# Optimization experiments

Measured on AMD Instinct MI355X. Metric: run time of the kernel, lower is better.

The kernel has to match this reference:

```python
import jax, jax.numpy as jnp
import numpy as np

EPS = 1e-5

def setup_inputs() -> dict:
    key = jax.random.key(0)
    ks = jax.random.split(key, 5)
    B, C, N, L = 32, 128, 4096, 6
    M = N // 8  # 512
    x = jax.random.normal(ks[0], (B, C, N, 1), dtype=jnp.float32)
    # small init scale keeps softmax logits in a sane range
    W_pool = jax.random.normal(ks[1], (M, C), dtype=jnp.float32) * 0.05
    Wf = jax.random.normal(ks[2], (L, M, M), dtype=jnp.float32) * 0.02
    gamma = jnp.ones((L, M), dtype=jnp.float32)
    beta = jnp.zeros((L, M), dtype=jnp.float32)
    W_unpool = jax.random.normal(ks[3], (M, C), dtype=jnp.float32) * 0.05
    b_unpool = jnp.zeros((M,), dtype=jnp.float32)
    return {"x": x, "W_pool": W_pool, "Wf": Wf, "gamma": gamma,
            "beta": beta, "W_unpool": W_unpool, "b_unpool": b_unpool}


def reference(x, W_pool, Wf, gamma, beta, W_unpool, b_unpool):
    # x: [B, C, N, 1]
    xs = x[..., 0]  # [B, C, N]
    # ---- Pool_1_to_1: 1x1 conv C->M, softmax over N, weighted sum ----
    Spool = jax.nn.softmax(jnp.einsum('mc,bcn->bmn', W_pool, xs), axis=2)
    h = jnp.einsum('bcn,bmn->bmc', xs, Spool)  # pooled then transposed: [B, M, C]
    # ---- n_layers of Order_Aware_Filtering_1_to_1 on [B, M, C] (channels=M) ----
    L = Wf.shape[0]
    for l in range(L):
        y = jnp.einsum('om,bmc->boc', Wf[l], h)  # 1x1 conv M->M
        mu = jnp.mean(y, axis=(0, 2), keepdims=True)          # BN over (B, spatial)
        var = jnp.mean((y - mu) ** 2, axis=(0, 2), keepdims=True)  # biased var
        yn = (y - mu) * jax.lax.rsqrt(var + EPS)
        yn = yn * gamma[l][None, :, None] + beta[l][None, :, None]
        h = jax.nn.relu(yn + h)  # residual + non-lin
    x1 = jnp.transpose(h, (0, 2, 1))  # [B, C, M]
    # ---- Unpool_1_to_1: 1x1 conv (with bias) C->M, softmax over M ----
    ul = jnp.einsum('mc,bcn->bmn', W_unpool, xs) + b_unpool[None, :, None]
    Sun = jax.nn.softmax(ul, axis=1)
    out = jnp.einsum('bcm,bmn->bcn', x1, Sun)
    return out[..., None]  # [B, C, N, 1]
```

## Files before the change

kernel.cpp:

```cpp
#include <hip/hip_runtime.h>
#include <hip/hip_bf16.h>

typedef float f32x4 __attribute__((ext_vector_type(4)));
typedef __bf16 bf16_t;
typedef __bf16 bf16x4 __attribute__((ext_vector_type(4)));
typedef __bf16 bf16x8 __attribute__((ext_vector_type(8)));

#define MFMA16(a, b, c) __builtin_amdgcn_mfma_f32_16x16x32_bf16(a, b, c, 0, 0, 0)

constexpr int C_ = 128;
constexpr int N_ = 4096;
constexpr int M_ = 512;
constexpr int NL = 6;

#define NEG_INF (-__builtin_huge_valf())

constexpr int XST = 136;
constexpr int NSTP = 40;
constexpr int PSTU = 72;

__global__ __launch_bounds__(256) void k_wsplit(const float* __restrict__ W,
                                                bf16_t* __restrict__ hi,
                                                bf16_t* __restrict__ lo) {
  const size_t i4 = ((size_t)blockIdx.x * 256 + threadIdx.x) * 4;
  f32x4 v = *(const f32x4*)&W[i4];
  bf16x4 h4, l4;
#pragma unroll
  for (int k = 0; k < 4; ++k) {
    bf16_t h = (bf16_t)v[k];
    h4[k] = h;
    l4[k] = (bf16_t)(v[k] - (float)h);
  }
  *(bf16x4*)&hi[i4] = h4;
  *(bf16x4*)&lo[i4] = l4;
}

__global__ __launch_bounds__(256) void k_wfsplit(const float* __restrict__ W,
                                                 bf16_t* __restrict__ hi,
                                                 bf16_t* __restrict__ lo) {
  const size_t i4 = ((size_t)blockIdx.x * 256 + threadIdx.x) * 4;
  const int l = (int)(i4 >> 18);
  const int rem = (int)(i4 & 262143);
  const int o = rem >> 9, m = rem & 511;
  f32x4 v = *(const f32x4*)&W[i4];
  bf16x4 h4, l4;
#pragma unroll
  for (int k = 0; k < 4; ++k) {
    bf16_t h = (bf16_t)v[k];
    h4[k] = h;
    l4[k] = (bf16_t)(v[k] - (float)h);
  }
  const size_t ad = (((size_t)l * 16 + (m >> 5)) * 512 + o) * 32 + (m & 31);
  *(bf16x4*)&hi[ad] = h4;
  *(bf16x4*)&lo[ad] = l4;
}

__global__ __launch_bounds__(256) void k_wusplit(const float* __restrict__ W,
                                                 bf16_t* __restrict__ hi,
                                                 bf16_t* __restrict__ lo) {
  const size_t i4 = ((size_t)blockIdx.x * 256 + threadIdx.x) * 4;
  const int m = (int)(i4 >> 7), c = (int)(i4 & 127);
  f32x4 v = *(const f32x4*)&W[i4];
  bf16x4 h4, l4;
#pragma unroll
  for (int k = 0; k < 4; ++k) {
    bf16_t h = (bf16_t)v[k];
    h4[k] = h;
    l4[k] = (bf16_t)(v[k] - (float)h);
  }
  const size_t ad = ((size_t)(c >> 5) * 512 + m) * 32 + (c & 31);
  *(bf16x4*)&hi[ad] = h4;
  *(bf16x4*)&lo[ad] = l4;
}

__global__ __launch_bounds__(256) void k_xsplit(const float* __restrict__ xs,
                                                bf16_t* __restrict__ thi,
                                                bf16_t* __restrict__ tlo) {
  __shared__ float T[128 * 68];
  const int n0 = blockIdx.x * 64, b = blockIdx.y;
  const int t = threadIdx.x;
  const float* xsb = xs + (size_t)b * C_ * N_;
#pragma unroll
  for (int i = 0; i < 8; ++i) {
    int slot = i * 256 + t;
    int c = slot >> 4, n4 = (slot & 15) * 4;
    *(f32x4*)&T[c * 68 + n4] = *(const f32x4*)&xsb[(size_t)c * N_ + n0 + n4];
  }
  __syncthreads();
  const int n = t >> 2, cb = (t & 3) * 32;
  bf16x8 h8[4], l8[4];
#pragma unroll
  for (int g = 0; g < 4; ++g)
#pragma unroll
    for (int j = 0; j < 8; ++j) {
      float v = T[(cb + g * 8 + j) * 68 + n];
      bf16_t hh = (bf16_t)v;
      h8[g][j] = hh;
      l8[g][j] = (bf16_t)(v - (float)hh);
    }
  const size_t base = ((size_t)b * N_ + n0 + n) * C_ + cb;
#pragma unroll
  for (int g = 0; g < 4; ++g) {
    *(bf16x8*)&thi[base + g * 8] = h8[g];
    *(bf16x8*)&tlo[base + g * 8] = l8[g];
  }
}

__global__ __launch_bounds__(256) void k_pool(const bf16_t* __restrict__ xsThi,
                                              const bf16_t* __restrict__ xsTlo,
                                              const float* __restrict__ x,
                                              const bf16_t* __restrict__ Wph,
                                              const bf16_t* __restrict__ Wpl,
                                              float* __restrict__ h_part,
                                              float* __restrict__ ml) {
  __shared__ bf16_t XH[32 * XST], XL[32 * XST];
  __shared__ bf16_t XCH[128 * NSTP], XCL[128 * NSTP];
  const int d = blockIdx.x;
  const int lin = ((d & 7) << 7) | (d >> 3);
  const int b = lin >> 5, r5 = lin & 31;
  const int mt = r5 >> 2, seg = r5 & 3;
  const int m0 = mt * 64;
  const int t = threadIdx.x, w = t >> 6, lane = t & 63, l15 = lane & 15, q = lane >> 4;

  const int sn0 = t >> 4, sn1 = (256 + t) >> 4;
  const int scg = (t & 15) * 8;
  const size_t sgb = ((size_t)b * N_ + seg * 1024) * C_ + scg;
  const int xc = t >> 3, xn4 = (t & 7) * 4;
  const float* xb = x + (size_t)b * C_ * N_;

  bf16x8 aWh[4], aWl[4];
#pragma unroll
  for (int k = 0; k < 4; ++k) {
    const size_t ra = (size_t)(m0 + w * 16 + l15) * C_ + k * 32 + q * 8;
    aWh[k] = *(const bf16x8*)&Wph[ra];
    aWl[k] = *(const bf16x8*)&Wpl[ra];
  }

  f32x4 acc[8];
#pragma unroll
  for (int cs = 0; cs < 8; ++cs) acc[cs] = f32x4{0.f, 0.f, 0.f, 0.f};
  float lsum = 0.f;

  for (int ch = 0; ch < 32; ++ch) {
    const int n0g = seg * 1024 + ch * 32;
    const size_t off = sgb + (size_t)ch * 32 * C_;
    __syncthreads();
    bf16x8 th0 = *(const bf16x8*)&xsThi[off + (size_t)sn0 * C_];
    bf16x8 th1 = *(const bf16x8*)&xsThi[off + (size_t)sn1 * C_];
    bf16x8 tl0 = *(const bf16x8*)&xsTlo[off + (size_t)sn0 * C_];
    bf16x8 tl1 = *(const bf16x8*)&xsTlo[off + (size_t)sn1 * C_];
    f32x4 xv[4];
#pragma unroll
    for (int i = 0; i < 4; ++i) {
      const int c = xc + i * 32;
      xv[i] = *(const f32x4*)&xb[(size_t)c * N_ + n0g + xn4];
    }
    *(bf16x8*)&XH[sn0 * XST + scg] = th0;
    *(bf16x8*)&XH[sn1 * XST + scg] = th1;
    *(bf16x8*)&XL[sn0 * XST + scg] = tl0;
    *(bf16x8*)&XL[sn1 * XST + scg] = tl1;
#pragma unroll
    for (int i = 0; i < 4; ++i) {
      const int c = xc + i * 32;
      bf16x4 h4, l4;
#pragma unroll
      for (int j = 0; j < 4; ++j) {
        bf16_t hh = (bf16_t)xv[i][j];
        h4[j] = hh;
        l4[j] = (bf16_t)(xv[i][j] - (float)hh);
      }
      *(bf16x4*)&XCH[c * NSTP + xn4] = h4;
      *(bf16x4*)&XCL[c * NSTP + xn4] = l4;
    }
    __syncthreads();

    f32x4 U0 = f32x4{0.f, 0.f, 0.f, 0.f}, U1 = f32x4{0.f, 0.f, 0.f, 0.f};
#pragma unroll
    for (int k = 0; k < 4; ++k) {
      {
        const int o = l15 * XST + k * 32 + q * 8;
        bf16x8 bh = *(const bf16x8*)&XH[o];
        bf16x8 bl = *(const bf16x8*)&XL[o];
        U0 = MFMA16(bh, aWh[k], U0);
        U0 = MFMA16(bl, aWh[k], U0);
        U0 = MFMA16(bh, aWl[k], U0);
      }
      {
        const int o = (16 + l15) * XST + k * 32 + q * 8;
        bf16x8 bh = *(const bf16x8*)&XH[o];
        bf16x8 bl = *(const bf16x8*)&XL[o];
        U1 = MFMA16(bh, aWh[k], U1);
        U1 = MFMA16(bl, aWh[k], U1);
        U1 = MFMA16(bh, aWl[k], U1);
      }
    }

    f32x4 pe0, pe1;
#pragma unroll
    for (int r = 0; r < 4; ++r) {
      pe0[r] = __expf(U0[r]);
      pe1[r] = __expf(U1[r]);
      lsum += pe0[r] + pe1[r];
    }

    const int slo = l15 + ((lane & 16) ? 32 : 0);
    float pj[8];
#pragma unroll
    for (int r = 0; r < 4; ++r) {
      float a0 = __shfl(pe0[r], slo);
      float a1 = __shfl(pe1[r], slo);
      pj[r] = (q & 2) ? a1 : a0;
      float b0 = __shfl(pe0[r], slo + 16);
      float b1 = __shfl(pe1[r], slo + 16);
      pj[4 + r] = (q & 2) ? b1 : b0;
    }
    bf16x8 aPh, aPl;
#pragma unroll
    for (int j = 0; j < 8; ++j) {
      bf16_t hh = (bf16_t)pj[j];
      aPh[j] = hh;
      aPl[j] = (bf16_t)(pj[j] - (float)hh);
    }

#pragma unroll
    for (int cs = 0; cs < 8; ++cs) {
      const int ob = (cs * 16 + l15) * NSTP + q * 8;
      bf16x8 bh = *(const bf16x8*)&XCH[ob];
      bf16x8 bl = *(const bf16x8*)&XCL[ob];
      acc[cs] = MFMA16(aPh, bh, acc[cs]);
      acc[cs] = MFMA16(aPh, bl, acc[cs]);
      acc[cs] = MFMA16(aPl, bh, acc[cs]);
    }
  }

  const size_t sb = (size_t)seg * 32 + b;
  lsum += __shfl_xor(lsum, 16);
  lsum += __shfl_xor(lsum, 32);
  if (lane < 16) ml[sb * 512 + m0 + w * 16 + lane] = lsum;
#pragma unroll
  for (int cs = 0; cs < 8; ++cs)
#pragma unroll
    for (int r = 0; r < 4; ++r) {
      const int m = m0 + w * 16 + q * 4 + r;
      h_part[(sb * 512 + m) * 128 + cs * 16 + l15] = acc[cs][r];
    }
}

__global__ __launch_bounds__(128) void k_combine(const float* __restrict__ h_part,
                                                 const float* __restrict__ ml,
                                                 float* __restrict__ hbuf) {
  const int mb = blockIdx.x;
  const int m = mb >> 5, b = mb & 31;
  const int c = threadIdx.x;
  float L = 0.f, acc = 0.f;
#pragma unroll
  for (int s = 0; s < 4; ++s) {
    L += ml[((size_t)s * 32 + b) * 512 + m];
    acc += h_part[(((size_t)s * 32 + b) * 512 + m) * 128 + c];
  }
  hbuf[(size_t)m * 4096 + b * 128 + c] = acc / L;
}

__global__ __launch_bounds__(256) void k_hsplit(const float* __restrict__ h,
                                                bf16_t* __restrict__ thi,
                                                bf16_t* __restrict__ tlo) {
  __shared__ float T[64 * 65];
  const int m0 = blockIdx.x * 64, c0 = blockIdx.y * 64;
  const int t = threadIdx.x;
#pragma unroll
  for (int ii = 0; ii < 4; ++ii) {
    int slot = ii * 256 + t;
    int m = slot >> 4, c4 = (slot & 15) * 4;
    f32x4 v = *(const f32x4*)&h[(size_t)(m0 + m) * 4096 + c0 + c4];
#pragma unroll
    for (int k = 0; k < 4; ++k) T[(c4 + k) * 65 + m] = v[k];
  }
  __syncthreads();
  const int row = t >> 2, mg = (t & 3) * 16;
  const int bc = c0 + row, bb = bc >> 7, cc = bc & 127;
#pragma unroll
  for (int half = 0; half < 2; ++half) {
    bf16x8 h8, l8;
#pragma unroll
    for (int j = 0; j < 8; ++j) {
      float v = T[row * 65 + mg + half * 8 + j];
      bf16_t hh = (bf16_t)v;
      h8[j] = hh;
      l8[j] = (bf16_t)(v - (float)hh);
    }
    const int m8 = m0 + mg + half * 8;
    const size_t ad = (((size_t)bb * 16 + (m8 >> 5)) * 128 + cc) * 32 + (m8 & 31);
    *(bf16x8*)&thi[ad] = h8;
    *(bf16x8*)&tlo[ad] = l8;
  }
}

__global__ __launch_bounds__(256) void k_bnsplit(const float* __restrict__ ybuf,
                                                 float* __restrict__ hbuf,
                                                 const float* __restrict__ stats,
                                                 const float* __restrict__ gamma,
                                                 const float* __restrict__ beta,
                                                 int l,
                                                 bf16_t* __restrict__ thi,
                                                 bf16_t* __restrict__ tlo) {
  __shared__ float T[64 * 65];
  const int m0 = blockIdx.x * 64, c0 = blockIdx.y * 64;
  const int t = threadIdx.x;
#pragma unroll
  for (int ii = 0; ii < 4; ++ii) {
    int slot = ii * 256 + t;
    int m = slot >> 4, c4 = (slot & 15) * 4;
    const int o = m0 + m;
    const float mu = stats[l * 1024 + o] * (1.f / 4096.f);
    const float var = stats[l * 1024 + 512 + o] * (1.f / 4096.f) - mu * mu;
    const float rs = rsqrtf(var + 1e-5f);
    const float g = gamma[l * 512 + o];
    const float bt = beta[l * 512 + o];
    const size_t gidx = (size_t)o * 4096 + c0 + c4;
    f32x4 y = *(const f32x4*)&ybuf[gidx];
    f32x4 h = *(const f32x4*)&hbuf[gidx];
    f32x4 r;
#pragma unroll
    for (int k = 0; k < 4; ++k) {
      r[k] = fmaxf((y[k] - mu) * rs * g + bt + h[k], 0.f);
      T[(c4 + k) * 65 + m] = r[k];
    }
    *(f32x4*)&hbuf[gidx] = r;
  }
  __syncthreads();
  const int row = t >> 2, mg = (t & 3) * 16;
  const int bc = c0 + row, bb = bc >> 7, cc = bc & 127;
#pragma unroll
  for (int half = 0; half < 2; ++half) {
    bf16x8 h8, l8;
#pragma unroll
    for (int j = 0; j < 8; ++j) {
      float v = T[row * 65 + mg + half * 8 + j];
      bf16_t hh = (bf16_t)v;
      h8[j] = hh;
      l8[j] = (bf16_t)(v - (float)hh);
    }
    const int m8 = m0 + mg + half * 8;
    const size_t ad = (((size_t)bb * 16 + (m8 >> 5)) * 128 + cc) * 32 + (m8 & 31);
    *(bf16x8*)&thi[ad] = h8;
    *(bf16x8*)&tlo[ad] = l8;
  }
}

__global__ __launch_bounds__(256) void k_layerA(const bf16_t* __restrict__ Whi,
                                                const bf16_t* __restrict__ Wlo,
                                                const bf16_t* __restrict__ hThi,
                                                const bf16_t* __restrict__ hTlo,
                                                int l, float* __restrict__ ybuf,
                                                float* __restrict__ stats) {
  const int o0 = blockIdx.x * 32;
  const int bb = blockIdx.y;
  const int t = threadIdx.x;
  const int w = t >> 6, lane = t & 63, l15 = lane & 15, q = lane >> 4;
  const int bcw = bb * 128 + w * 32;

  f32x4 acc[2][2];
#pragma unroll
  for (int i = 0; i < 2; ++i)
#pragma unroll
    for (int j = 0; j < 2; ++j) acc[i][j] = f32x4{0.f, 0.f, 0.f, 0.f};

  for (int k0 = 0; k0 < M_; k0 += 32) {
    const int mb = k0 >> 5;
    bf16x8 ah[2], al[2], bh[2], bl[2];
#pragma unroll
    for (int os = 0; os < 2; ++os) {
      const size_t ro =
          (((size_t)l * 16 + mb) * 512 + o0 + os * 16 + l15) * 32 + q * 8;
      ah[os] = *(const bf16x8*)&Whi[ro];
      al[os] = *(const bf16x8*)&Wlo[ro];
    }
#pragma unroll
    for (int ns = 0; ns < 2; ++ns) {
      const size_t rb =
          (((size_t)bb * 16 + mb) * 128 + w * 32 + ns * 16 + l15) * 32 + q * 8;
      bh[ns] = *(const bf16x8*)&hThi[rb];
      bl[ns] = *(const bf16x8*)&hTlo[rb];
    }
#pragma unroll
    for (int os = 0; os < 2; ++os)
#pragma unroll
      for (int ns = 0; ns < 2; ++ns) {
        acc[os][ns] = MFMA16(ah[os], bh[ns], acc[os][ns]);
        acc[os][ns] = MFMA16(ah[os], bl[ns], acc[os][ns]);
        acc[os][ns] = MFMA16(al[os], bh[ns], acc[os][ns]);
      }
  }

  float s1[2][4], s2[2][4];
#pragma unroll
  for (int os = 0; os < 2; ++os)
#pragma unroll
    for (int r = 0; r < 4; ++r) {
      float a = 0.f, b2 = 0.f;
#pragma unroll
      for (int ns = 0; ns < 2; ++ns) {
        float v = acc[os][ns][r];
        ybuf[(size_t)(o0 + os * 16 + q * 4 + r) * 4096 + bcw + ns * 16 + l15] = v;
        a += v;
        b2 += v * v;
      }
      s1[os][r] = a;
      s2[os][r] = b2;
    }
#pragma unroll
  for (int os = 0; os < 2; ++os)
#pragma unroll
    for (int r = 0; r < 4; ++r) {
#pragma unroll
      for (int off = 1; off < 16; off <<= 1) {
        s1[os][r] += __shfl_xor(s1[os][r], off);
        s2[os][r] += __shfl_xor(s2[os][r], off);
      }
      if (l15 == 0) {
        const int o = o0 + os * 16 + q * 4 + r;
        atomicAdd(&stats[l * 1024 + o], s1[os][r]);
        atomicAdd(&stats[l * 1024 + 512 + o], s2[os][r]);
      }
    }
}

__global__ __launch_bounds__(256) void k_unpool(const bf16_t* __restrict__ xsThi,
                                                const bf16_t* __restrict__ xsTlo,
                                                const bf16_t* __restrict__ Wuh,
                                                const bf16_t* __restrict__ Wul,
                                                const float* __restrict__ bun,
                                                const bf16_t* __restrict__ x1hi,
                                                const bf16_t* __restrict__ x1lo,
                                                float* __restrict__ out) {
  __shared__ bf16_t XH[64 * XST], XL[64 * XST];
  __shared__ bf16_t PH[64 * PSTU], PL[64 * PSTU];
  __shared__ float colsum_s[4][64];
  __shared__ float L_s[64];
  const int n0 = blockIdx.x * 64, b = blockIdx.y;
  const int t = threadIdx.x, w = t >> 6, lane = t & 63, l15 = lane & 15, q = lane >> 4;

#pragma unroll
  for (int i = 0; i < 4; ++i) {
    int slot = i * 256 + t;
    int n = slot >> 4, cg = (slot & 15) * 8;
    const size_t g = ((size_t)b * N_ + n0 + n) * C_ + cg;
    *(bf16x8*)&XH[n * XST + cg] = *(const bf16x8*)&xsThi[g];
    *(bf16x8*)&XL[n * XST + cg] = *(const bf16x8*)&xsTlo[g];
  }
  colsum_s[w][lane] = 0.f;
  f32x4 acc[2][4];
#pragma unroll
  for (int cs = 0; cs < 2; ++cs)
#pragma unroll
    for (int nt = 0; nt < 4; ++nt) acc[cs][nt] = f32x4{0.f, 0.f, 0.f, 0.f};
  __syncthreads();

  for (int ch = 0; ch < 8; ++ch) {
    const int mg0 = ch * 64 + w * 16;
    f32x4 U[4];
#pragma unroll
    for (int nt = 0; nt < 4; ++nt) U[nt] = f32x4{0.f, 0.f, 0.f, 0.f};
#pragma unroll
    for (int k = 0; k < 4; ++k) {
      const size_t ra = ((size_t)k * 512 + mg0 + l15) * 32 + q * 8;
      bf16x8 ah = *(const bf16x8*)&Wuh[ra];
      bf16x8 al = *(const bf16x8*)&Wul[ra];
#pragma unroll
      for (int nt = 0; nt < 4; ++nt) {
        const int o = (nt * 16 + l15) * XST + k * 32 + q * 8;
        bf16x8 bh = *(const bf16x8*)&XH[o];
        bf16x8 bl = *(const bf16x8*)&XL[o];
        U[nt] = MFMA16(ah, bh, U[nt]);
        U[nt] = MFMA16(ah, bl, U[nt]);
        U[nt] = MFMA16(al, bh, U[nt]);
      }
    }
    float bi[4];
#pragma unroll
    for (int r = 0; r < 4; ++r) bi[r] = bun[mg0 + q * 4 + r];

#pragma unroll
    for (int nt = 0; nt < 4; ++nt) {
      bf16x4 ph4, pl4;
      float s = 0.f;
#pragma unroll
      for (int r = 0; r < 4; ++r) {
        float pv = __expf(U[nt][r] + bi[r]);
        s += pv;
        bf16_t hh = (bf16_t)pv;
        ph4[r] = hh;
        pl4[r] = (bf16_t)(pv - (float)hh);
      }
      s += __shfl_xor(s, 16);
      s += __shfl_xor(s, 32);
      if (lane < 16) colsum_s[w][nt * 16 + lane] += s;
      const int o = (nt * 16 + l15) * PSTU + w * 16 + q * 4;
      *(bf16x4*)&PH[o] = ph4;
      *(bf16x4*)&PL[o] = pl4;
    }
    __syncthreads();

#pragma unroll
    for (int ks = 0; ks < 2; ++ks) {
      bf16x8 ah2[2], al2[2];
#pragma unroll
      for (int cs = 0; cs < 2; ++cs) {
        const size_t ga =
            (((size_t)b * 16 + ch * 2 + ks) * 128 + w * 32 + cs * 16 + l15) * 32 +
            q * 8;
        ah2[cs] = *(const bf16x8*)&x1hi[ga];
        al2[cs] = *(const bf16x8*)&x1lo[ga];
      }
#pragma unroll
      for (int nt = 0; nt < 4; ++nt) {
        const int o = (nt * 16 + l15) * PSTU + ks * 32 + q * 8;
        bf16x8 bh = *(const bf16x8*)&PH[o];
        bf16x8 bl = *(const bf16x8*)&PL[o];
#pragma unroll
        for (int cs = 0; cs < 2; ++cs) {
          acc[cs][nt] = MFMA16(ah2[cs], bh, acc[cs][nt]);
          acc[cs][nt] = MFMA16(ah2[cs], bl, acc[cs][nt]);
          acc[cs][nt] = MFMA16(al2[cs], bh, acc[cs][nt]);
        }
      }
    }
    __syncthreads();
  }
  if (t < 64)
    L_s[t] = colsum_s[0][t] + colsum_s[1][t] + colsum_s[2][t] + colsum_s[3][t];
  __syncthreads();
#pragma unroll
  for (int nt = 0; nt < 4; ++nt) {
    const float invL = 1.f / L_s[nt * 16 + l15];
#pragma unroll
    for (int cs = 0; cs < 2; ++cs) {
      const int c = w * 32 + cs * 16 + q * 4;
#pragma unroll
      for (int r = 0; r < 4; ++r)
        out[((size_t)b * 128 + c + r) * (size_t)N_ + n0 + nt * 16 + l15] =
            acc[cs][nt][r] * invL;
    }
  }
}

extern "C" void kernel_launch(void* const* d_in, const int* in_sizes, int n_in,
                              void* d_out, int out_size, void* d_ws, size_t ws_size,
                              hipStream_t stream) {
  const float* x = (const float*)d_in[0];
  const float* W_pool = (const float*)d_in[1];
  const float* Wf = (const float*)d_in[2];
  const float* gamma = (const float*)d_in[3];
  const float* beta = (const float*)d_in[4];
  const float* W_unpool = (const float*)d_in[5];
  const float* b_unpool = (const float*)d_in[6];
  float* out = (float*)d_out;

  char* ws = (char*)d_ws;
  float* h_part = (float*)ws; ws += (size_t)4 * 32 * 512 * 128 * 4;
  float* ml = (float*)ws;     ws += (size_t)4 * 32 * 512 * 4;
  float* hbuf = (float*)ws;   ws += (size_t)512 * 4096 * 4;
  float* stats = (float*)ws;  ws += NL * 1024 * 4;
  bf16_t* xsThi = (bf16_t*)ws; ws += (size_t)32 * N_ * C_ * 2;
  bf16_t* xsTlo = (bf16_t*)ws; ws += (size_t)32 * N_ * C_ * 2;
  bf16_t* Wuh = (bf16_t*)ws;  ws += (size_t)M_ * C_ * 2;
  bf16_t* Wul = (bf16_t*)ws;  ws += (size_t)M_ * C_ * 2;
  bf16_t* Wph = (bf16_t*)ws;  ws += (size_t)M_ * C_ * 2;
  bf16_t* Wpl = (bf16_t*)ws;  ws += (size_t)M_ * C_ * 2;
  bf16_t* Whi = (bf16_t*)ws;  ws += (size_t)NL * M_ * M_ * 2;
  bf16_t* Wlo = (bf16_t*)ws;  ws += (size_t)NL * M_ * M_ * 2;
  char* hp = (char*)h_part;
  float* ybuf = (float*)(hp);
  bf16_t* hThi = (bf16_t*)(hp + 8388608);
  bf16_t* hTlo = (bf16_t*)(hp + 12582912);

  hipMemsetAsync(stats, 0, NL * 1024 * 4, stream);
  k_xsplit<<<dim3(64, 32), 256, 0, stream>>>(x, xsThi, xsTlo);
  k_wsplit<<<dim3(64), 256, 0, stream>>>(W_pool, Wph, Wpl);
  k_wusplit<<<dim3(64), 256, 0, stream>>>(W_unpool, Wuh, Wul);
  k_wfsplit<<<dim3(1536), 256, 0, stream>>>(Wf, Whi, Wlo);
  k_pool<<<dim3(1024), 256, 0, stream>>>(xsThi, xsTlo, x, Wph, Wpl,
                                         h_part, ml);
  k_combine<<<dim3(16384), 128, 0, stream>>>(h_part, ml, hbuf);
  k_hsplit<<<dim3(8, 64), 256, 0, stream>>>(hbuf, hThi, hTlo);
  for (int l = 0; l < NL; ++l) {
    k_layerA<<<dim3(16, 32), 256, 0, stream>>>(Whi, Wlo, hThi, hTlo, l, ybuf, stats);
    k_bnsplit<<<dim3(8, 64), 256, 0, stream>>>(ybuf, hbuf, stats, gamma, beta, l,
                                               hThi, hTlo);
  }
  k_unpool<<<dim3(64, 32), 256, 0, stream>>>(xsThi, xsTlo, Wuh, Wul, b_unpool,
                                             hThi, hTlo, out);
}
```

Measured before the change: 700.2 us.

## Double-buffer shared tiles in pool and unpool kernels to overlap loads with MFMA

In the pool kernel, shared X tiles become ping-pong buffers. The next chunk's global loads are issued before the current chunk's MFMA work and stored to the alternate buffer afterwards, which removes one barrier per iteration. The x loads are also widened to 8 floats per thread. In the unpool kernel, the P tiles are double-buffered so the trailing barrier can go, and the x1 operand loads are hoisted to the top of each chunk. The aim is to hide global latency behind compute, at the cost of more LDS and registers, which may lower occupancy.

```diff
diff --git a/kernel.cpp b/kernel.cpp
--- a/kernel.cpp
+++ b/kernel.cpp
@@ -113,8 +113,8 @@
                                               const bf16_t* __restrict__ Wpl,
                                               float* __restrict__ h_part,
                                               float* __restrict__ ml) {
-  __shared__ bf16_t XH[32 * XST], XL[32 * XST];
-  __shared__ bf16_t XCH[128 * NSTP], XCL[128 * NSTP];
+  __shared__ bf16_t XH2[2][32 * XST], XL2[2][32 * XST];
+  __shared__ bf16_t XCH2[2][128 * NSTP], XCL2[2][128 * NSTP];
   const int d = blockIdx.x;
   const int lin = ((d & 7) << 7) | (d >> 3);
   const int b = lin >> 5, r5 = lin & 31;
@@ -125,7 +125,7 @@
   const int sn0 = t >> 4, sn1 = (256 + t) >> 4;
   const int scg = (t & 15) * 8;
   const size_t sgb = ((size_t)b * N_ + seg * 1024) * C_ + scg;
-  const int xc = t >> 3, xn4 = (t & 7) * 4;
+  const int xc2 = t >> 2, xn8 = (t & 3) * 8;
   const float* xb = x + (size_t)b * C_ * N_;
 
   bf16x8 aWh[4], aWl[4];
@@ -141,38 +141,63 @@
   for (int cs = 0; cs < 8; ++cs) acc[cs] = f32x4{0.f, 0.f, 0.f, 0.f};
   float lsum = 0.f;
 
+  bf16x8 th0, th1, tl0, tl1;
+  float xf[2][8];
+
+  {
+    const size_t off = sgb;
+    th0 = *(const bf16x8*)&xsThi[off + (size_t)sn0 * C_];
+    th1 = *(const bf16x8*)&xsThi[off + (size_t)sn1 * C_];
+    tl0 = *(const bf16x8*)&xsTlo[off + (size_t)sn0 * C_];
+    tl1 = *(const bf16x8*)&xsTlo[off + (size_t)sn1 * C_];
+#pragma unroll
+    for (int i = 0; i < 2; ++i) {
+      const int c = xc2 + i * 64;
+      *(f32x4*)&xf[i][0] = *(const f32x4*)&xb[(size_t)c * N_ + seg * 1024 + xn8];
+      *(f32x4*)&xf[i][4] = *(const f32x4*)&xb[(size_t)c * N_ + seg * 1024 + xn8 + 4];
+    }
+    *(bf16x8*)&XH2[0][sn0 * XST + scg] = th0;
+    *(bf16x8*)&XH2[0][sn1 * XST + scg] = th1;
+    *(bf16x8*)&XL2[0][sn0 * XST + scg] = tl0;
+    *(bf16x8*)&XL2[0][sn1 * XST + scg] = tl1;
+#pragma unroll
+    for (int i = 0; i < 2; ++i) {
+      const int c = xc2 + i * 64;
+      bf16x8 h8, l8;
+#pragma unroll
+      for (int j = 0; j < 8; ++j) {
+        bf16_t hh = (bf16_t)xf[i][j];
+        h8[j] = hh;
+        l8[j] = (bf16_t)(xf[i][j] - (float)hh);
+      }
+      *(bf16x8*)&XCH2[0][c * NSTP + xn8] = h8;
+      *(bf16x8*)&XCL2[0][c * NSTP + xn8] = l8;
+    }
+  }
+
+  int p = 0;
   for (int ch = 0; ch < 32; ++ch) {
-    const int n0g = seg * 1024 + ch * 32;
-    const size_t off = sgb + (size_t)ch * 32 * C_;
     __syncthreads();
-    bf16x8 th0 = *(const bf16x8*)&xsThi[off + (size_t)sn0 * C_];
-    bf16x8 th1 = *(const bf16x8*)&xsThi[off + (size_t)sn1 * C_];
-    bf16x8 tl0 = *(const bf16x8*)&xsTlo[off + (size_t)sn0 * C_];
-    bf16x8 tl1 = *(const bf16x8*)&xsTlo[off + (size_t)sn1 * C_];
-    f32x4 xv[4];
-#pragma unroll
-    for (int i = 0; i < 4; ++i) {
-      const int c = xc + i * 32;
-      xv[i] = *(const f32x4*)&xb[(size_t)c * N_ + n0g + xn4];
-    }
-    *(bf16x8*)&XH[sn0 * XST + scg] = th0;
-    *(bf16x8*)&XH[sn1 * XST + scg] = th1;
-    *(bf16x8*)&XL[sn0 * XST + scg] = tl0;
-    *(bf16x8*)&XL[sn1 * XST + scg] = tl1;
-#pragma unroll
-    for (int i = 0; i < 4; ++i) {
-      const int c = xc + i * 32;
-      bf16x4 h4, l4;
-#pragma unroll
-      for (int j = 0; j < 4; ++j) {
-        bf16_t hh = (bf16_t)xv[i][j];
-        h4[j] = hh;
-        l4[j] = (bf16_t)(xv[i][j] - (float)hh);
-      }
-      *(bf16x4*)&XCH[c * NSTP + xn4] = h4;
-      *(bf16x4*)&XCL[c * NSTP + xn4] = l4;
-    }
-    __syncthreads();
+
+    if (ch < 31) {
+      const int nn = seg * 1024 + (ch + 1) * 32;
+      const size_t off = sgb + (size_t)(ch + 1) * 32 * C_;
+      th0 = *(const bf16x8*)&xsThi[off + (size_t)sn0 * C_];
+      th1 = *(const bf16x8*)&xsThi[off + (size_t)sn1 * C_];
+      tl0 = *(const bf16x8*)&xsTlo[off + (size_t)sn0 * C_];
+      tl1 = *(const bf16x8*)&xsTlo[off + (size_t)sn1 * C_];
+#pragma unroll
+      for (int i = 0; i < 2; ++i) {
+        const int c = xc2 + i * 64;
+        *(f32x4*)&xf[i][0] = *(const f32x4*)&xb[(size_t)c * N_ + nn + xn8];
+        *(f32x4*)&xf[i][4] = *(const f32x4*)&xb[(size_t)c * N_ + nn + xn8 + 4];
+      }
+    }
+
+    const bf16_t* XH = &XH2[p][0];
+    const bf16_t* XL = &XL2[p][0];
+    const bf16_t* XCH = &XCH2[p][0];
+    const bf16_t* XCL = &XCL2[p][0];
 
     f32x4 U0 = f32x4{0.f, 0.f, 0.f, 0.f}, U1 = f32x4{0.f, 0.f, 0.f, 0.f};
 #pragma unroll
@@ -231,6 +256,28 @@
       acc[cs] = MFMA16(aPh, bl, acc[cs]);
       acc[cs] = MFMA16(aPl, bh, acc[cs]);
     }
+
+    if (ch < 31) {
+      const int pn = p ^ 1;
+      *(bf16x8*)&XH2[pn][sn0 * XST + scg] = th0;
+      *(bf16x8*)&XH2[pn][sn1 * XST + scg] = th1;
+      *(bf16x8*)&XL2[pn][sn0 * XST + scg] = tl0;
+      *(bf16x8*)&XL2[pn][sn1 * XST + scg] = tl1;
+#pragma unroll
+      for (int i = 0; i < 2; ++i) {
+        const int c = xc2 + i * 64;
+        bf16x8 h8, l8;
+#pragma unroll
+        for (int j = 0; j < 8; ++j) {
+          bf16_t hh = (bf16_t)xf[i][j];
+          h8[j] = hh;
+          l8[j] = (bf16_t)(xf[i][j] - (float)hh);
+        }
+        *(bf16x8*)&XCH2[pn][c * NSTP + xn8] = h8;
+        *(bf16x8*)&XCL2[pn][c * NSTP + xn8] = l8;
+      }
+    }
+    p ^= 1;
   }
 
   const size_t sb = (size_t)seg * 32 + b;
@@ -434,7 +481,7 @@
                                                 const bf16_t* __restrict__ x1lo,
                                                 float* __restrict__ out) {
   __shared__ bf16_t XH[64 * XST], XL[64 * XST];
-  __shared__ bf16_t PH[64 * PSTU], PL[64 * PSTU];
+  __shared__ bf16_t PH2[2][64 * PSTU], PL2[2][64 * PSTU];
   __shared__ float colsum_s[4][64];
   __shared__ float L_s[64];
   const int n0 = blockIdx.x * 64, b = blockIdx.y;
@@ -456,8 +503,22 @@
     for (int nt = 0; nt < 4; ++nt) acc[cs][nt] = f32x4{0.f, 0.f, 0.f, 0.f};
   __syncthreads();
 
+  int p = 0;
   for (int ch = 0; ch < 8; ++ch) {
     const int mg0 = ch * 64 + w * 16;
+
+    bf16x8 xah[2][2], xal[2][2];
+#pragma unroll
+    for (int ks = 0; ks < 2; ++ks)
+#pragma unroll
+      for (int cs = 0; cs < 2; ++cs) {
+        const size_t ga =
+            (((size_t)b * 16 + ch * 2 + ks) * 128 + w * 32 + cs * 16 + l15) * 32 +
+            q * 8;
+        xah[ks][cs] = *(const bf16x8*)&x1hi[ga];
+        xal[ks][cs] = *(const bf16x8*)&x1lo[ga];
+      }
+
     f32x4 U[4];
 #pragma unroll
     for (int nt = 0; nt < 4; ++nt) U[nt] = f32x4{0.f, 0.f, 0.f, 0.f};
@@ -496,37 +557,29 @@
       s += __shfl_xor(s, 32);
       if (lane < 16) colsum_s[w][nt * 16 + lane] += s;
       const int o = (nt * 16 + l15) * PSTU + w * 16 + q * 4;
-      *(bf16x4*)&PH[o] = ph4;
-      *(bf16x4*)&PL[o] = pl4;
+      *(bf16x4*)&PH2[p][o] = ph4;
+      *(bf16x4*)&PL2[p][o] = pl4;
     }
     __syncthreads();
 
 #pragma unroll
     for (int ks = 0; ks < 2; ++ks) {
-      bf16x8 ah2[2], al2[2];
-#pragma unroll
-      for (int cs = 0; cs < 2; ++cs) {
-        const size_t ga =
-            (((size_t)b * 16 + ch * 2 + ks) * 128 + w * 32 + cs * 16 + l15) * 32 +
-            q * 8;
-        ah2[cs] = *(const bf16x8*)&x1hi[ga];
-        al2[cs] = *(const bf16x8*)&x1lo[ga];
-      }
 #pragma unroll
       for (int nt = 0; nt < 4; ++nt) {
         const int o = (nt * 16 + l15) * PSTU + ks * 32 + q * 8;
-        bf16x8 bh = *(const bf16x8*)&PH[o];
-        bf16x8 bl = *(const bf16x8*)&PL[o];
+        bf16x8 bh = *(const bf16x8*)&PH2[p][o];
+        bf16x8 bl = *(const bf16x8*)&PL2[p][o];
 #pragma unroll
         for (int cs = 0; cs < 2; ++cs) {
-          acc[cs][nt] = MFMA16(ah2[cs], bh, acc[cs][nt]);
-          acc[cs][nt] = MFMA16(ah2[cs], bl, acc[cs][nt]);
-          acc[cs][nt] = MFMA16(al2[cs], bh, acc[cs][nt]);
+          acc[cs][nt] = MFMA16(xah[ks][cs], bh, acc[cs][nt]);
+          acc[cs][nt] = MFMA16(xah[ks][cs], bl, acc[cs][nt]);
+          acc[cs][nt] = MFMA16(xal[ks][cs], bh, acc[cs][nt]);
         }
       }
     }
-    __syncthreads();
-  }
+    p ^= 1;
+  }
+  __syncthreads();
   if (t < 64)
     L_s[t] = colsum_s[0][t] + colsum_s[1][t] + colsum_s[2][t] + colsum_s[3][t];
   __syncthreads();
```

Result: faster. 663.9 us (-5.2%).
